# Kernel optimization log

Hardware: AMD Instinct MI355X
Metric: run time of the kernel (lower is better)

Reference implementation:

```python
import jax, jax.numpy as jnp
import numpy as np
import math

FACTOR = 5  # ProbAttention factor


def setup_inputs() -> dict:
    key = jax.random.key(0)
    kq, kk, kv = jax.random.split(key, 3)
    B, L, H, D = 4, 2048, 8, 64
    return {
        "queries": jax.random.normal(kq, (B, L, H, D), dtype=jnp.float32),
        "keys": jax.random.normal(kk, (B, L, H, D), dtype=jnp.float32),
        "values": jax.random.normal(kv, (B, L, H, D), dtype=jnp.float32),
    }


def reference(queries, keys, values):
    # queries/keys/values: [B, L, H, D] (self-attention, L == S)
    B, L, H, D = queries.shape
    S = keys.shape[1]
    Q = jnp.transpose(queries, (0, 2, 1, 3))  # [B,H,L,D]
    K = jnp.transpose(keys, (0, 2, 1, 3))     # [B,H,S,D]
    V = jnp.transpose(values, (0, 2, 1, 3))   # [B,H,S,D]

    # U: number of top queries kept; u: number of sampled keys per query
    n_top = min(max(1, int(FACTOR * math.log(max(S, 2)))), S, L)
    sample_k = min(max(1, int(FACTOR * math.log(max(L, 2)))), S)

    # --- _prob_QK: sampled QK, sparsity measure, top-k query selection ---
    idx_key = jax.random.key(42)  # matches torch.randint(L, (S, sample_k)) role
    index_sample = jax.random.randint(idx_key, (L, sample_k), 0, S)  # [L_Q, sample_k]
    K_sample = K[:, :, index_sample, :]                # [B,H,L,sample_k,D]
    QK_sample = jnp.einsum('bhqd,bhqjd->bhqj', Q, K_sample)  # [B,H,L,sample_k]
    # sparsity measure: max - mean (mean over full key length L_K = S)
    M = QK_sample.max(axis=-1) - QK_sample.sum(axis=-1) / S   # [B,H,L]
    M_top = jax.lax.top_k(M, n_top)[1]                 # [B,H,n_top] query indices
    Q_reduce = jnp.take_along_axis(Q, M_top[..., None], axis=2)  # [B,H,n_top,D]
    scores = jnp.einsum('bhud,bhkd->bhuk', Q_reduce, K)          # [B,H,n_top,S]

    scale = 1.0 / math.sqrt(D)
    scores = scores * scale

    # --- initial context: mask_flag=True and L_Q == L_V -> causal cumsum of V ---
    context = jnp.cumsum(V, axis=2)                    # [B,H,L,D]

    # --- masked softmax over selected queries (ProbMask: causal triu(1) rows) ---
    tri = jnp.triu(jnp.ones((S, S), dtype=bool), 1)    # [S,S]
    mask = tri[M_top]                                  # [B,H,n_top,S]
    scores = jnp.where(mask, -jnp.inf, scores)
    attn = jax.nn.softmax(scores, axis=-1)             # dropout is identity at eval
    attended = jnp.einsum('bhuk,bhkd->bhud', attn, V)  # [B,H,n_top,D]

    # --- scatter attended values into context at selected query positions ---
    b_idx = jnp.arange(B)[:, None, None]
    h_idx = jnp.arange(H)[None, :, None]
    context = context.at[b_idx, h_idx, M_top].set(attended)

    return jnp.transpose(context, (0, 2, 1, 3))        # [B,L,H,D]
```

## Files before the change

kernel.cpp:

```cpp
#include <hip/hip_runtime.h>
#include <hip/hip_bf16.h>
#include <math.h>

#define B_   4
#define L_   2048
#define H_   8
#define D_   64
#define NTOP 38
#define SAMPK 38


#define WS_M_OFF    0
#define WS_MTOP_OFF 262144
#define WS_SMALL    (WS_MTOP_OFF + 4864)
#define NSLOT16     (B_ * H_ * NTOP * 16)
#define WS16_PMAX   WS_SMALL
#define WS16_PSUM   (WS16_PMAX + NSLOT16 * 4)
#define WS16_PPV    (WS16_PSUM + NSLOT16 * 4)
#define WS16_TOTAL  (WS16_PPV + NSLOT16 * D_ * 4)

#define CHUNK16 128
#define SPITCH  132

__device__ __forceinline__ uint32_t rotl32(uint32_t v, int d) {
  return (v << d) | (v >> (32 - d));
}

__device__ __forceinline__ void threefry2x32(uint32_t k0, uint32_t k1,
                                             uint32_t x0, uint32_t x1,
                                             uint32_t& y0, uint32_t& y1) {
  const uint32_t ks2 = k0 ^ k1 ^ 0x1BD11BDAu;
  const uint32_t ks[3] = {k0, k1, ks2};
  x0 += k0; x1 += k1;
  const int ra[4] = {13, 15, 26, 6};
  const int rb[4] = {17, 29, 16, 24};
#pragma unroll
  for (int g = 0; g < 5; ++g) {
    const int* r = (g & 1) ? rb : ra;
#pragma unroll
    for (int i = 0; i < 4; ++i) {
      x0 += x1;
      x1 = rotl32(x1, r[i]);
      x1 ^= x0;
    }
    x0 += ks[(g + 1) % 3];
    x1 += ks[(g + 2) % 3] + (uint32_t)(g + 1);
  }
  y0 = x0; y1 = x1;
}

__device__ __forceinline__ int sample_idx(int t) {
  uint32_t k2_0, k2_1, y0, y1;
  threefry2x32(0u, 42u, 0u, 1u, k2_0, k2_1);
  threefry2x32(k2_0, k2_1, 0u, (uint32_t)t, y0, y1);
  return (int)((y0 ^ y1) & 2047u);
}

__device__ __forceinline__ int sample_idx_k2(uint32_t k2_0, uint32_t k2_1, int t) {
  uint32_t y0, y1;
  threefry2x32(k2_0, k2_1, 0u, (uint32_t)t, y0, y1);
  return (int)((y0 ^ y1) & 2047u);
}

__device__ __forceinline__ int argmax32_low(const float* __restrict__ vals,
                                            float& bv_out) {
  float t[16];
#pragma unroll
  for (int i = 0; i < 16; ++i) t[i] = fmaxf(vals[2 * i], vals[2 * i + 1]);
#pragma unroll
  for (int i = 0; i < 8; ++i) t[i] = fmaxf(t[2 * i], t[2 * i + 1]);
#pragma unroll
  for (int i = 0; i < 4; ++i) t[i] = fmaxf(t[2 * i], t[2 * i + 1]);
  float bv = fmaxf(fmaxf(t[0], t[1]), fmaxf(t[2], t[3]));
  uint32_t msk = 0u;
#pragma unroll
  for (int i = 0; i < 32; ++i)
    msk |= (vals[i] == bv) ? (1u << i) : 0u;
  bv_out = bv;
  return __ffs(msk) - 1;
}

__device__ __forceinline__ void topk38_wave_lds(const float* __restrict__ Mrow,
                                                int lane, int* __restrict__ spos,
                                                int* __restrict__ mtop_g, bool writeG) {
  float vals[32];
#pragma unroll
  for (int i = 0; i < 32; ++i)
    vals[i] = Mrow[lane + 64 * i];

  for (int u = 0; u < NTOP; ++u) {
    float bv;
    int bslot = argmax32_low(vals, bv);
    float v = bv;
    int idx = lane + 64 * bslot;
#pragma unroll
    for (int off = 1; off < 64; off <<= 1) {
      float v2 = __shfl_xor(v, off);
      int   i2 = __shfl_xor(idx, off);
      if (v2 > v || (v2 == v && i2 < idx)) { v = v2; idx = i2; }
    }
    if (lane == 0) {
      spos[u] = idx;
      if (writeG) mtop_g[u] = idx;
    }
    if ((idx & 63) == lane) {
      int slot = idx >> 6;
#pragma unroll
      for (int i = 0; i < 32; ++i)
        if (i == slot) vals[i] = -1e38f;
    }
  }
}

__device__ __forceinline__ void topk38_wave(const float* __restrict__ Mrow,
                                            int lane, int* __restrict__ mrow_out) {
  float vals[32];
#pragma unroll
  for (int i = 0; i < 32; ++i)
    vals[i] = Mrow[lane + 64 * i];

  for (int u = 0; u < NTOP; ++u) {
    float bv;
    int bslot = argmax32_low(vals, bv);
    float v = bv;
    int idx = lane + 64 * bslot;
#pragma unroll
    for (int off = 1; off < 64; off <<= 1) {
      float v2 = __shfl_xor(v, off);
      int   i2 = __shfl_xor(idx, off);
      if (v2 > v || (v2 == v && i2 < idx)) { v = v2; idx = i2; }
    }
    if (lane == 0) mrow_out[u] = idx;
    if ((idx & 63) == lane) {
      int slot = idx >> 6;
#pragma unroll
      for (int i = 0; i < 32; ++i)
        if (i == slot) vals[i] = -1e38f;
    }
  }
}

__global__ __launch_bounds__(256) void m_cumsum_kernel(const float* __restrict__ Q,
                                                       const float* __restrict__ K,
                                                       const float* __restrict__ V,
                                                       float* __restrict__ M,
                                                       float* __restrict__ out) {
  __shared__ uint16_t sidx[16][SAMPK];
  __shared__ float cs[8][32];

  int tid = threadIdx.x;

  if (blockIdx.x < 64) {
    int bI = blockIdx.x;
    int bh = bI >> 1, dhalf = bI & 1;
    int h = bh & (H_ - 1), b = bh >> 3;
    int dl = tid & 31, c = tid >> 5;
    const int CH = L_ / 8;
    int d = dhalf * 32 + dl;
    size_t base = ((size_t)b * L_ * H_ + h) * D_ + d;
    const size_t ls = (size_t)H_ * D_;
    float s = 0.f;
    for (int l = c * CH; l < (c + 1) * CH; ++l)
      s += V[base + (size_t)l * ls];
    cs[c][dl] = s;
    __syncthreads();
    float run = 0.f;
    for (int cc = 0; cc < c; ++cc) run += cs[cc][dl];
    for (int l = c * CH; l < (c + 1) * CH; ++l) {
      run += V[base + (size_t)l * ls];
      out[base + (size_t)l * ls] = run;
    }
    return;
  }

  int bI = blockIdx.x - 64;
  int j8 = bI >> 3;
  int bh = (bI & 7) + 8 * (j8 >> 7);
  int chunk = j8 & 127;
  int grp = tid >> 4, c = tid & 15;
  int q = chunk * 16 + grp;
  int h = bh & (H_ - 1), b = bh >> 3;

  {
    uint32_t k2_0, k2_1;
    threefry2x32(0u, 42u, 0u, 1u, k2_0, k2_1);
    for (int s = tid; s < 16 * SAMPK; s += 256) {
      int ql = s / SAMPK, jj = s - ql * SAMPK;
      sidx[ql][jj] =
          (uint16_t)sample_idx_k2(k2_0, k2_1, (chunk * 16 + ql) * SAMPK + jj);
    }
  }
  __syncthreads();

  float4 qv = *(const float4*)(Q + (((size_t)b * L_ + q) * H_ + h) * D_ + 4 * c);
  const float* Kbase = K + ((size_t)b * L_ * H_ + h) * D_ + 4 * c;

  float mx = -1e30f, smv = 0.f;
  int j = 0;
  for (; j + 4 <= SAMPK; j += 4) {
    int r0 = (int)sidx[grp][j];
    int r1 = (int)sidx[grp][j + 1];
    int r2 = (int)sidx[grp][j + 2];
    int r3 = (int)sidx[grp][j + 3];
    float4 k0 = *(const float4*)(Kbase + (size_t)r0 * (H_ * D_));
    float4 k1 = *(const float4*)(Kbase + (size_t)r1 * (H_ * D_));
    float4 k2 = *(const float4*)(Kbase + (size_t)r2 * (H_ * D_));
    float4 k3 = *(const float4*)(Kbase + (size_t)r3 * (H_ * D_));
    float p0 = qv.x * k0.x + qv.y * k0.y + qv.z * k0.z + qv.w * k0.w;
    float p1 = qv.x * k1.x + qv.y * k1.y + qv.z * k1.z + qv.w * k1.w;
    float p2 = qv.x * k2.x + qv.y * k2.y + qv.z * k2.z + qv.w * k2.w;
    float p3 = qv.x * k3.x + qv.y * k3.y + qv.z * k3.z + qv.w * k3.w;
#pragma unroll
    for (int off = 1; off < 16; off <<= 1) {
      p0 += __shfl_xor(p0, off);
      p1 += __shfl_xor(p1, off);
      p2 += __shfl_xor(p2, off);
      p3 += __shfl_xor(p3, off);
    }
    mx = fmaxf(mx, p0); smv += p0;
    mx = fmaxf(mx, p1); smv += p1;
    mx = fmaxf(mx, p2); smv += p2;
    mx = fmaxf(mx, p3); smv += p3;
  }
  for (; j < SAMPK; ++j) {
    int r0 = (int)sidx[grp][j];
    float4 k0 = *(const float4*)(Kbase + (size_t)r0 * (H_ * D_));
    float p0 = qv.x * k0.x + qv.y * k0.y + qv.z * k0.z + qv.w * k0.w;
#pragma unroll
    for (int off = 1; off < 16; off <<= 1)
      p0 += __shfl_xor(p0, off);
    mx = fmaxf(mx, p0); smv += p0;
  }
  if (c == 0)
    M[(size_t)bh * L_ + q] = mx - smv * (1.0f / (float)L_);
}

__global__ __launch_bounds__(512) void attn_split_tk_kernel(const float* __restrict__ Q,
                                                            const float* __restrict__ K,
                                                            const float* __restrict__ V,
                                                            const float* __restrict__ M,
                                                            int* __restrict__ mtop,
                                                            float* __restrict__ pmax,
                                                            float* __restrict__ psum,
                                                            float* __restrict__ ppv) {
  __shared__ float4 sK[CHUNK16 * 16];
  __shared__ float  sS[NTOP * SPITCH];
  __shared__ float4 sQ[NTOP * 16];
  __shared__ int    spos[NTOP];

  int bI = blockIdx.x;
  int c = bI & 15;
  int bh = bI >> 4;
  int h = bh & (H_ - 1), b = bh >> 3;
  int kstart = c * CHUNK16;
  int tid = threadIdx.x;

  const float* Kb = K + ((size_t)b * L_ * H_ + h) * D_;
  const float* Vb = V + ((size_t)b * L_ * H_ + h) * D_;
  const float* Qb = Q + ((size_t)b * L_ * H_ + h) * D_;

  if (tid < 64) {
    topk38_wave_lds(M + (size_t)bh * L_, tid, spos, mtop + bh * NTOP, c == 0);
  } else {
    for (int s = tid - 64; s < CHUNK16 * 16; s += 448) {
      int row = s >> 4, f = s & 15;
      sK[row * 16 + (f ^ (row & 15))] =
          *(const float4*)(Kb + (size_t)(kstart + row) * (H_ * D_) + 4 * f);
    }
  }
  __syncthreads();

  int maxpos = 0;
  for (int u = 0; u < NTOP; ++u) maxpos = max(maxpos, spos[u]);
  if (maxpos < kstart) return;

  for (int s = tid; s < NTOP * 16; s += 512) {
    int u = s >> 4, f = s & 15;
    sQ[s] = *(const float4*)(Qb + (size_t)spos[u] * (H_ * D_) + 4 * f);
  }
  __syncthreads();

  {
    int k = tid & 127;
    int ug = tid >> 7;
    float4 kreg[16];
#pragma unroll
    for (int f = 0; f < 16; ++f)
      kreg[f] = sK[k * 16 + (f ^ (k & 15))];

    int u0 = ug * 10, u1 = min(NTOP, u0 + 10);
    for (int u = u0; u < u1; ++u) {
      int pos = spos[u];
      if (pos < kstart) continue;
      int kloc = pos - kstart;
      float dot = 0.f;
#pragma unroll
      for (int f = 0; f < 16; ++f) {
        float4 qf = sQ[u * 16 + f];
        dot += kreg[f].x * qf.x + kreg[f].y * qf.y
             + kreg[f].z * qf.z + kreg[f].w * qf.w;
      }
      sS[u * SPITCH + k] = (k <= kloc) ? dot * 0.125f : -1e30f;
    }
  }
  __syncthreads();

  int w = tid >> 6, lane = tid & 63;
  int kq = lane >> 4, dq = lane & 15;
  for (int u = w; u < NTOP; u += 8) {
    int pos = spos[u];
    if (pos < kstart) continue;
    int kcnt = min(CHUNK16, pos + 1 - kstart);

    float s0 = sS[u * SPITCH + lane];
    float s1 = sS[u * SPITCH + 64 + lane];
    float m = fmaxf(s0, s1);
#pragma unroll
    for (int off = 1; off < 64; off <<= 1)
      m = fmaxf(m, __shfl_xor(m, off));
    float p0 = expf(s0 - m), p1 = expf(s1 - m);
    sS[u * SPITCH + lane] = p0;
    sS[u * SPITCH + 64 + lane] = p1;
    float sum = p0 + p1;
#pragma unroll
    for (int off = 1; off < 64; off <<= 1)
      sum += __shfl_xor(sum, off);

    float4 acc = make_float4(0.f, 0.f, 0.f, 0.f);
    for (int k0 = 0; k0 < kcnt; k0 += 4) {
      int kk = k0 + kq;
      if (kk < kcnt) {
        float p = sS[u * SPITCH + kk];
        float4 v4 = *(const float4*)(Vb + (size_t)(kstart + kk) * (H_ * D_) + 4 * dq);
        acc.x += p * v4.x; acc.y += p * v4.y;
        acc.z += p * v4.z; acc.w += p * v4.w;
      }
    }
    acc.x += __shfl_xor(acc.x, 16); acc.y += __shfl_xor(acc.y, 16);
    acc.z += __shfl_xor(acc.z, 16); acc.w += __shfl_xor(acc.w, 16);
    acc.x += __shfl_xor(acc.x, 32); acc.y += __shfl_xor(acc.y, 32);
    acc.z += __shfl_xor(acc.z, 32); acc.w += __shfl_xor(acc.w, 32);

    int slot = (bh * NTOP + u) * 16 + c;
    if (lane < 16)
      *(float4*)(ppv + (size_t)slot * D_ + 4 * lane) = acc;
    if (lane == 0) { pmax[slot] = m; psum[slot] = sum; }
  }
}

template <int NCHT>
__global__ __launch_bounds__(64) void attn_fin_kernel(const float* __restrict__ pmax,
                                                      const float* __restrict__ psum,
                                                      const float* __restrict__ ppv,
                                                      const int* __restrict__ mtop,
                                                      float* __restrict__ out) {
  const int CH = L_ / NCHT;
  int uu = blockIdx.x;
  int bh = uu / NTOP;
  int h = bh & (H_ - 1), b = bh >> 3;
  int pos = mtop[uu];
  if (pos < 0) pos = 0;
  if (pos > L_ - 1) pos = L_ - 1;
  int klen = pos + 1;
  int nch = (klen + CH - 1) / CH;
  int tid = threadIdx.x;

  int base = uu * NCHT;
  float gmax = -1e30f;
#pragma unroll
  for (int cc = 0; cc < NCHT; ++cc)
    if (cc < nch) gmax = fmaxf(gmax, pmax[base + cc]);

  float gsum = 0.f, acc = 0.f;
#pragma unroll
  for (int cc = 0; cc < NCHT; ++cc) {
    if (cc < nch) {
      float w0 = expf(pmax[base + cc] - gmax);
      gsum += psum[base + cc] * w0;
      acc += ppv[(size_t)(base + cc) * D_ + tid] * w0;
    }
  }
  out[(((size_t)b * L_ + pos) * H_ + h) * D_ + tid] = acc / gsum;
}

__global__ __launch_bounds__(256) void m_kernel(const float* __restrict__ Q,
                                                const float* __restrict__ K,
                                                float* __restrict__ M) {
  int bI = blockIdx.x;
  int j8 = bI >> 3;
  int bh = (bI & 7) + 8 * (j8 >> 7);
  int chunk = j8 & 127;
  int tid = threadIdx.x;
  int grp = tid >> 4, c = tid & 15;
  int q = chunk * 16 + grp;
  int h = bh & (H_ - 1), b = bh >> 3;

  __shared__ uint16_t sidx[16][SAMPK];
  for (int s = tid; s < 16 * SAMPK; s += 256) {
    int ql = s / SAMPK, jj = s - ql * SAMPK;
    sidx[ql][jj] = (uint16_t)sample_idx((chunk * 16 + ql) * SAMPK + jj);
  }
  __syncthreads();

  float4 qv = *(const float4*)(Q + (((size_t)b * L_ + q) * H_ + h) * D_ + 4 * c);
  const float* Kbase = K + ((size_t)b * L_ * H_ + h) * D_ + 4 * c;

  float mx = -1e30f, smv = 0.f;
  for (int j = 0; j < SAMPK; ++j) {
    int row = (int)sidx[grp][j];
    float4 kv = *(const float4*)(Kbase + (size_t)row * (H_ * D_));
    float part = qv.x * kv.x + qv.y * kv.y + qv.z * kv.z + qv.w * kv.w;
#pragma unroll
    for (int off = 1; off < 16; off <<= 1)
      part += __shfl_xor(part, off);
    mx = fmaxf(mx, part);
    smv += part;
  }
  if (c == 0)
    M[(size_t)bh * L_ + q] = mx - smv * (1.0f / (float)L_);
}

__global__ __launch_bounds__(1024) void cumsum_kernel(const float* __restrict__ V,
                                                      float* __restrict__ out) {
  int bI = blockIdx.x;
  int bh = bI >> 1, dhalf = bI & 1;
  int h = bh & (H_ - 1), b = bh >> 3;
  int tid = threadIdx.x;
  int dl = tid & 31, c = tid >> 5;
  int d = dhalf * 32 + dl;
  const int CH = L_ / 32;
  __shared__ float cs[32][32];
  size_t base = ((size_t)b * L_ * H_ + h) * D_ + d;
  const size_t ls = (size_t)H_ * D_;
  float s = 0.f;
  for (int l = c * CH; l < (c + 1) * CH; ++l)
    s += V[base + (size_t)l * ls];
  cs[c][dl] = s;
// ... 108 lines not shown
                                                    float* __restrict__ out) {
  int bh = blockIdx.x;
  int h = bh % H_, b = bh / H_;
  int tid = threadIdx.x;

  __shared__ float sm[L_];
  __shared__ float redv[256];
  __shared__ int   redi[256];
  __shared__ int   mtop_s[NTOP];
  __shared__ float qs[D_];
  __shared__ float part[4][D_];

  for (int q = tid; q < L_; q += 256) {
    const float4* q4 = (const float4*)(Q + (((size_t)b * L_ + q) * H_ + h) * D_);
    float4 qv[16];
#pragma unroll
    for (int i = 0; i < 16; ++i) qv[i] = q4[i];
    float mx = -1e30f, smv = 0.f;
    for (int j = 0; j < SAMPK; ++j) {
      int kk = sample_idx(q * SAMPK + j);
      const float4* k4 = (const float4*)(K + (((size_t)b * L_ + kk) * H_ + h) * D_);
      float dot = 0.f;
#pragma unroll
      for (int i = 0; i < 16; ++i) {
        float4 kv = k4[i];
        dot += qv[i].x * kv.x + qv[i].y * kv.y + qv[i].z * kv.z + qv[i].w * kv.w;
      }
      mx = fmaxf(mx, dot);
      smv += dot;
    }
    sm[q] = mx - smv * (1.0f / (float)L_);
  }
  __syncthreads();

  for (int u = 0; u < NTOP; ++u) {
    float bv = -1e38f; int bi = -1;
    for (int i = tid; i < L_; i += 256) {
      float v = sm[i];
      if (v > bv) { bv = v; bi = i; }
    }
    redv[tid] = bv; redi[tid] = bi;
    __syncthreads();
    for (int s = 128; s > 0; s >>= 1) {
      if (tid < s) {
        float v2 = redv[tid + s]; int i2 = redi[tid + s];
        if (v2 > redv[tid] ||
            (v2 == redv[tid] && i2 >= 0 && (redi[tid] < 0 || i2 < redi[tid]))) {
          redv[tid] = v2; redi[tid] = i2;
        }
      }
      __syncthreads();
    }
    if (tid == 0) {
      int sel = redi[0];
      if (sel < 0) sel = 0;
      mtop_s[u] = sel;
      sm[sel] = -1e38f;
    }
    __syncthreads();
  }

  for (int u = 0; u < NTOP; ++u) {
    int pos = mtop_s[u];
    if (pos < 0) pos = 0;
    if (pos > L_ - 1) pos = L_ - 1;
    int klen = pos + 1;

    __syncthreads();
    if (tid < D_)
      qs[tid] = Q[(((size_t)b * L_ + pos) * H_ + h) * D_ + tid];
    __syncthreads();

    float lmax = -1e30f;
    for (int k = tid; k < klen; k += 256) {
      const float4* k4 = (const float4*)(K + (((size_t)b * L_ + k) * H_ + h) * D_);
      float dot = 0.f;
#pragma unroll
      for (int i = 0; i < 16; ++i) {
        float4 kv = k4[i];
        dot += qs[4 * i] * kv.x + qs[4 * i + 1] * kv.y
             + qs[4 * i + 2] * kv.z + qs[4 * i + 3] * kv.w;
      }
      dot *= 0.125f;
      sm[k] = dot;
      lmax = fmaxf(lmax, dot);
    }
    redv[tid] = lmax;
    __syncthreads();
    for (int s = 128; s > 0; s >>= 1) {
      if (tid < s) redv[tid] = fmaxf(redv[tid], redv[tid + s]);
      __syncthreads();
    }
    float mx = redv[0];
    __syncthreads();

    float lsum = 0.f;
    for (int k = tid; k < klen; k += 256) {
      float p = expf(sm[k] - mx);
      sm[k] = p;
      lsum += p;
    }
    redv[tid] = lsum;
    __syncthreads();
    for (int s = 128; s > 0; s >>= 1) {
      if (tid < s) redv[tid] += redv[tid + s];
      __syncthreads();
    }
    float inv = 1.0f / redv[0];
    __syncthreads();

    int d = tid & 63, slice = tid >> 6;
    float acc = 0.f;
    for (int k = slice; k < klen; k += 4)
      acc += sm[k] * V[(((size_t)b * L_ + k) * H_ + h) * D_ + d];
    part[slice][d] = acc;
    __syncthreads();
    if (tid < D_) {
      float r = (part[0][tid] + part[1][tid]) + (part[2][tid] + part[3][tid]);
      out[(((size_t)b * L_ + pos) * H_ + h) * D_ + tid] = r * inv;
    }
  }
}

extern "C" void kernel_launch(void* const* d_in, const int* in_sizes, int n_in,
                              void* d_out, int out_size, void* d_ws, size_t ws_size,
                              hipStream_t stream) {
  const float* Q = (const float*)d_in[0];
  const float* K = (const float*)d_in[1];
  const float* V = (const float*)d_in[2];
  float* out = (float*)d_out;

  if (ws_size >= (size_t)WS16_TOTAL) {
    char* ws = (char*)d_ws;
    float* M    = (float*)(ws + WS_M_OFF);
    int*   mt   = (int*)(ws + WS_MTOP_OFF);
    float* pmax = (float*)(ws + WS16_PMAX);
    float* psum = (float*)(ws + WS16_PSUM);
    float* ppv  = (float*)(ws + WS16_PPV);

    m_cumsum_kernel<<<4160, 256, 0, stream>>>(Q, K, V, M, out);
    attn_split_tk_kernel<<<B_ * H_ * 16, 512, 0, stream>>>(Q, K, V, M, mt,
                                                           pmax, psum, ppv);
    attn_fin_kernel<16><<<B_ * H_ * NTOP, 64, 0, stream>>>(pmax, psum, ppv, mt, out);
  } else if (ws_size >= (size_t)WS_SMALL) {
    char* ws = (char*)d_ws;
    float* M  = (float*)(ws + WS_M_OFF);
    int*   mt = (int*)(ws + WS_MTOP_OFF);

    m_kernel<<<4096, 256, 0, stream>>>(Q, K, M);
    topk_reg_kernel<<<B_ * H_, 64, 0, stream>>>(M, mt);
    cumsum_kernel<<<B_ * H_ * 2, 1024, 0, stream>>>(V, out);
    attn_kernel<<<B_ * H_ * NTOP, 256, 0, stream>>>(Q, K, V, mt, out);
  } else {
    cumsum_kernel<<<B_ * H_ * 2, 1024, 0, stream>>>(V, out);
    fused_kernel<<<B_ * H_, 256, 0, stream>>>(Q, K, V, out);
  }
}
```

Measured before the change: 200.2 us.

## Fuse all stages into one cooperative kernel with grid-wide syncs

Adds a persistent cooperative mega-kernel that runs cumsum, sampled-QK sparsity scoring, top-k selection, split-K attention over 64-key chunks and the final merge in a single launch, with grid.sync between phases. It removes the cost of three separate kernel launches and the gaps between them. The attention split also changes from 16 to 32 chunks, and chunks entirely beyond the largest selected position are skipped. In exchange, grid-wide barriers add overhead, most blocks sit idle during the top-k phase, and the path only runs when 1024 blocks of 512 threads can be co-resident, otherwise it falls back to the old kernels.

Measured after the change: 201.5 us. About the same (+0.6%).

```diff
diff --git a/kernel.cpp b/kernel.cpp
--- a/kernel.cpp
+++ b/kernel.cpp
@@ -1,6 +1,9 @@
 #include <hip/hip_runtime.h>
 #include <hip/hip_bf16.h>
+#include <hip/hip_cooperative_groups.h>
 #include <math.h>
+
+namespace cg = cooperative_groups;
 
 #define B_   4
 #define L_   2048
@@ -18,9 +21,17 @@
 #define WS16_PSUM   (WS16_PMAX + NSLOT16 * 4)
 #define WS16_PPV    (WS16_PSUM + NSLOT16 * 4)
 #define WS16_TOTAL  (WS16_PPV + NSLOT16 * D_ * 4)
+#define NSLOT32     (B_ * H_ * NTOP * 32)
+#define WS32_PMAX   WS_SMALL
+#define WS32_PSUM   (WS32_PMAX + NSLOT32 * 4)
+#define WS32_PPV    (WS32_PSUM + NSLOT32 * 4)
+#define WS32_TOTAL  (WS32_PPV + NSLOT32 * D_ * 4)
 
 #define CHUNK16 128
 #define SPITCH  132
+#define CHM     64
+#define NCHM    32
+#define SPM     68
 
 __device__ __forceinline__ uint32_t rotl32(uint32_t v, int d) {
   return (v << d) | (v >> (32 - d));
@@ -80,9 +91,8 @@
   return __ffs(msk) - 1;
 }
 
-__device__ __forceinline__ void topk38_wave_lds(const float* __restrict__ Mrow,
-                                                int lane, int* __restrict__ spos,
-                                                int* __restrict__ mtop_g, bool writeG) {
+__device__ __forceinline__ void topk38_wave(const float* __restrict__ Mrow,
+                                            int lane, int* __restrict__ mrow_out) {
   float vals[32];
 #pragma unroll
   for (int i = 0; i < 32; ++i)
@@ -99,10 +109,7 @@
       int   i2 = __shfl_xor(idx, off);
       if (v2 > v || (v2 == v && i2 < idx)) { v = v2; idx = i2; }
     }
-    if (lane == 0) {
-      spos[u] = idx;
-      if (writeG) mtop_g[u] = idx;
-    }
+    if (lane == 0) mrow_out[u] = idx;
     if ((idx & 63) == lane) {
       int slot = idx >> 6;
 #pragma unroll
@@ -112,8 +119,9 @@
   }
 }
 
-__device__ __forceinline__ void topk38_wave(const float* __restrict__ Mrow,
-                                            int lane, int* __restrict__ mrow_out) {
+__device__ __forceinline__ void topk38_wave_lds(const float* __restrict__ Mrow,
+                                                int lane, int* __restrict__ spos,
+                                                int* __restrict__ mtop_g, bool writeG) {
   float vals[32];
 #pragma unroll
   for (int i = 0; i < 32; ++i)
@@ -130,12 +138,246 @@
       int   i2 = __shfl_xor(idx, off);
       if (v2 > v || (v2 == v && i2 < idx)) { v = v2; idx = i2; }
     }
-    if (lane == 0) mrow_out[u] = idx;
+    if (lane == 0) {
+      spos[u] = idx;
+      if (writeG) mtop_g[u] = idx;
+    }
     if ((idx & 63) == lane) {
       int slot = idx >> 6;
 #pragma unroll
       for (int i = 0; i < 32; ++i)
         if (i == slot) vals[i] = -1e38f;
+    }
+  }
+}
+
+struct SharedA {
+  uint16_t sidx[2][16][SAMPK];
+  float    cs[2][8][32];
+};
+struct SharedC {
+  float4 sK[CHM * 16];
+  float  sS[NTOP * SPM];
+  float4 sQ[NTOP * 16];
+  int    spos[NTOP];
+};
+union SharedU { SharedA a; SharedC c; };
+
+__global__ __launch_bounds__(512, 8) void mega_kernel(
+    const float* __restrict__ Q, const float* __restrict__ K,
+    const float* __restrict__ V, float* __restrict__ M,
+    int* __restrict__ mtop, float* __restrict__ pmax,
+    float* __restrict__ psum, float* __restrict__ ppv,
+    float* __restrict__ out) {
+  cg::grid_group grid = cg::this_grid();
+  __shared__ SharedU sh;
+
+  int bI = blockIdx.x;
+  int tid = threadIdx.x;
+  int half = tid >> 8, htid = tid & 255;
+
+  if (bI < 32) {
+    int unit = bI * 2 + half;
+    int bh = unit >> 1, dhalf = unit & 1;
+    int h = bh & (H_ - 1), b = bh >> 3;
+    int dl = htid & 31, cc8 = htid >> 5;
+    const int CH = L_ / 8;
+    int d = dhalf * 32 + dl;
+    size_t base = ((size_t)b * L_ * H_ + h) * D_ + d;
+    const size_t ls = (size_t)H_ * D_;
+    float s = 0.f;
+    for (int l = cc8 * CH; l < (cc8 + 1) * CH; ++l)
+      s += V[base + (size_t)l * ls];
+    sh.a.cs[half][cc8][dl] = s;
+    __syncthreads();
+    float run = 0.f;
+    for (int c2 = 0; c2 < cc8; ++c2) run += sh.a.cs[half][c2][dl];
+    for (int l = cc8 * CH; l < (cc8 + 1) * CH; ++l) {
+      run += V[base + (size_t)l * ls];
+      out[base + (size_t)l * ls] = run;
+    }
+  }
+
+  {
+    uint32_t k2_0, k2_1;
+    threefry2x32(0u, 42u, 0u, 1u, k2_0, k2_1);
+    for (int r = 0; r < 2; ++r) {
+      int um = (bI & 7) + 8 * (((bI >> 3) * 2 + half) * 2 + r);
+      int j8 = um >> 3;
+      int bh = (um & 7) + 8 * (j8 >> 7);
+      int chunk = j8 & 127;
+      int grp = htid >> 4, c = htid & 15;
+      int q = chunk * 16 + grp;
+      int h = bh & (H_ - 1), b = bh >> 3;
+
+      __syncthreads();
+      for (int s = htid; s < 16 * SAMPK; s += 256) {
+        int ql = s / SAMPK, jj = s - ql * SAMPK;
+        sh.a.sidx[half][ql][jj] =
+            (uint16_t)sample_idx_k2(k2_0, k2_1, (chunk * 16 + ql) * SAMPK + jj);
+      }
+      __syncthreads();
+
+      float4 qv = *(const float4*)(Q + (((size_t)b * L_ + q) * H_ + h) * D_ + 4 * c);
+      const float* Kbase = K + ((size_t)b * L_ * H_ + h) * D_ + 4 * c;
+
+      float mx = -1e30f, smv = 0.f;
+      int j = 0;
+      for (; j + 4 <= SAMPK; j += 4) {
+        int r0 = (int)sh.a.sidx[half][grp][j];
+        int r1 = (int)sh.a.sidx[half][grp][j + 1];
+        int r2 = (int)sh.a.sidx[half][grp][j + 2];
+        int r3 = (int)sh.a.sidx[half][grp][j + 3];
+        float4 k0 = *(const float4*)(Kbase + (size_t)r0 * (H_ * D_));
+        float4 k1 = *(const float4*)(Kbase + (size_t)r1 * (H_ * D_));
+        float4 k2 = *(const float4*)(Kbase + (size_t)r2 * (H_ * D_));
+        float4 k3 = *(const float4*)(Kbase + (size_t)r3 * (H_ * D_));
+        float p0 = qv.x * k0.x + qv.y * k0.y + qv.z * k0.z + qv.w * k0.w;
+        float p1 = qv.x * k1.x + qv.y * k1.y + qv.z * k1.z + qv.w * k1.w;
+        float p2 = qv.x * k2.x + qv.y * k2.y + qv.z * k2.z + qv.w * k2.w;
+        float p3 = qv.x * k3.x + qv.y * k3.y + qv.z * k3.z + qv.w * k3.w;
+#pragma unroll
+        for (int off = 1; off < 16; off <<= 1) {
+          p0 += __shfl_xor(p0, off);
+          p1 += __shfl_xor(p1, off);
+          p2 += __shfl_xor(p2, off);
+          p3 += __shfl_xor(p3, off);
+        }
+        mx = fmaxf(mx, p0); smv += p0;
+        mx = fmaxf(mx, p1); smv += p1;
+        mx = fmaxf(mx, p2); smv += p2;
+        mx = fmaxf(mx, p3); smv += p3;
+      }
+      for (; j < SAMPK; ++j) {
+        int r0 = (int)sh.a.sidx[half][grp][j];
+        float4 k0 = *(const float4*)(Kbase + (size_t)r0 * (H_ * D_));
+        float p0 = qv.x * k0.x + qv.y * k0.y + qv.z * k0.z + qv.w * k0.w;
+#pragma unroll
+        for (int off = 1; off < 16; off <<= 1)
+          p0 += __shfl_xor(p0, off);
+        mx = fmaxf(mx, p0); smv += p0;
+      }
+      if (c == 0)
+        M[(size_t)bh * L_ + q] = mx - smv * (1.0f / (float)L_);
+    }
+  }
+  grid.sync();
+
+  if (bI >= 32 && bI < 64 && tid < 64)
+    topk38_wave(M + (size_t)(bI - 32) * L_, tid, mtop + (bI - 32) * NTOP);
+  grid.sync();
+
+  {
+    int bh = (bI & 7) + 8 * (bI >> 8);
+    int c = (bI >> 3) & 31;
+    int h = bh & (H_ - 1), b = bh >> 3;
+    int kstart = c * CHM;
+
+    if (tid < NTOP) sh.c.spos[tid] = mtop[bh * NTOP + tid];
+    __syncthreads();
+    int maxpos = 0;
+    for (int u = 0; u < NTOP; ++u) maxpos = max(maxpos, sh.c.spos[u]);
+
+    if (maxpos >= kstart) {
+      const float* Kb = K + ((size_t)b * L_ * H_ + h) * D_;
+      const float* Vb = V + ((size_t)b * L_ * H_ + h) * D_;
+      const float* Qb = Q + ((size_t)b * L_ * H_ + h) * D_;
+
+      for (int s = tid; s < CHM * 16; s += 512) {
+        int row = s >> 4, f = s & 15;
+        sh.c.sK[row * 16 + (f ^ (row & 15))] =
+            *(const float4*)(Kb + (size_t)(kstart + row) * (H_ * D_) + 4 * f);
+      }
+      for (int s = tid; s < NTOP * 16; s += 512) {
+        int u = s >> 4, f = s & 15;
+        sh.c.sQ[s] = *(const float4*)(Qb + (size_t)sh.c.spos[u] * (H_ * D_) + 4 * f);
+      }
+      __syncthreads();
+
+      {
+        int k = tid & 63, ug = tid >> 6;
+        float4 kreg[16];
+#pragma unroll
+        for (int f = 0; f < 16; ++f)
+          kreg[f] = sh.c.sK[k * 16 + (f ^ (k & 15))];
+        for (int u = ug; u < NTOP; u += 8) {
+          int pos = sh.c.spos[u];
+          if (pos < kstart) continue;
+          float dot = 0.f;
+#pragma unroll
+          for (int f = 0; f < 16; ++f) {
+            float4 qf = sh.c.sQ[u * 16 + f];
+            dot += kreg[f].x * qf.x + kreg[f].y * qf.y
+                 + kreg[f].z * qf.z + kreg[f].w * qf.w;
+          }
+          sh.c.sS[u * SPM + k] = (k <= pos - kstart) ? dot * 0.125f : -1e30f;
+        }
+      }
+      __syncthreads();
+
+      {
+        int w = tid >> 6, lane = tid & 63;
+        int kq = lane >> 4, dq = lane & 15;
+        for (int u = w; u < NTOP; u += 8) {
+          int pos = sh.c.spos[u];
+          if (pos < kstart) continue;
+          int kcnt = min(CHM, pos + 1 - kstart);
+          float s0 = sh.c.sS[u * SPM + lane];
+          float m = s0;
+#pragma unroll
+          for (int off = 1; off < 64; off <<= 1)
+            m = fmaxf(m, __shfl_xor(m, off));
+          float p0 = expf(s0 - m);
+          sh.c.sS[u * SPM + lane] = p0;
+          float sum = p0;
+#pragma unroll
+          for (int off = 1; off < 64; off <<= 1)
+            sum += __shfl_xor(sum, off);
+
+          float4 acc = make_float4(0.f, 0.f, 0.f, 0.f);
+          for (int k0 = 0; k0 < kcnt; k0 += 4) {
+            int kk = k0 + kq;
+            if (kk < kcnt) {
+              float p = sh.c.sS[u * SPM + kk];
+              float4 v4 = *(const float4*)(Vb + (size_t)(kstart + kk) * (H_ * D_) + 4 * dq);
+              acc.x += p * v4.x; acc.y += p * v4.y;
+              acc.z += p * v4.z; acc.w += p * v4.w;
+            }
+          }
+          acc.x += __shfl_xor(acc.x, 16); acc.y += __shfl_xor(acc.y, 16);
+          acc.z += __shfl_xor(acc.z, 16); acc.w += __shfl_xor(acc.w, 16);
+          acc.x += __shfl_xor(acc.x, 32); acc.y += __shfl_xor(acc.y, 32);
+          acc.z += __shfl_xor(acc.z, 32); acc.w += __shfl_xor(acc.w, 32);
+
+          int slot = (bh * NTOP + u) * NCHM + c;
+          if (lane < 16)
+            *(float4*)(ppv + (size_t)slot * D_ + 4 * lane) = acc;
+          if (lane == 0) { pmax[slot] = m; psum[slot] = sum; }
+        }
+      }
+    }
+  }
+  grid.sync();
+
+  {
+    int wid = bI * 8 + (tid >> 6);
+    int lane = tid & 63;
+    if (wid < B_ * H_ * NTOP) {
+      int bh = wid / NTOP;
+      int h = bh & (H_ - 1), b = bh >> 3;
+      int pos = mtop[wid];
+      int nch = (pos + CHM) / CHM;
+      int base = wid * NCHM;
+      float gmax = -1e30f;
+      for (int cc = 0; cc < nch; ++cc)
+        gmax = fmaxf(gmax, pmax[base + cc]);
+      float gsum = 0.f, acc = 0.f;
+      for (int cc = 0; cc < nch; ++cc) {
+        float w0 = expf(pmax[base + cc] - gmax);
+        gsum += psum[base + cc] * w0;
+        acc += ppv[(size_t)(base + cc) * D_ + lane] * w0;
+      }
+      out[(((size_t)b * L_ + pos) * H_ + h) * D_ + lane] = acc / gsum;
     }
   }
 }
@@ -675,6 +917,38 @@
   const float* V = (const float*)d_in[2];
   float* out = (float*)d_out;
 
+  if (ws_size >= (size_t)WS32_TOTAL) {
+    static int coop = -1;
+    if (coop < 0) {
+      int dev = 0;
+      (void)hipGetDevice(&dev);
+      int attr = 0;
+      (void)hipDeviceGetAttribute(&attr, hipDeviceAttributeCooperativeLaunch, dev);
+      int nb = 0;
+      hipError_t oe =
+          hipOccupancyMaxActiveBlocksPerMultiprocessor(&nb, mega_kernel, 512, 0);
+      hipDeviceProp_t prop;
+      hipError_t pe = hipGetDeviceProperties(&prop, dev);
+      coop = (attr && oe == hipSuccess && pe == hipSuccess &&
+              (long)nb * prop.multiProcessorCount >= 1024) ? 1 : 0;
+    }
+    if (coop == 1) {
+      char* ws = (char*)d_ws;
+      float* M    = (float*)(ws + WS_M_OFF);
+      int*   mt   = (int*)(ws + WS_MTOP_OFF);
+      float* pmax = (float*)(ws + WS32_PMAX);
+      float* psum = (float*)(ws + WS32_PSUM);
+      float* ppv  = (float*)(ws + WS32_PPV);
+      void* args[] = {(void*)&Q, (void*)&K, (void*)&V, (void*)&M, (void*)&mt,
+                      (void*)&pmax, (void*)&psum, (void*)&ppv, (void*)&out};
+      hipError_t e = hipLaunchCooperativeKernel(mega_kernel, dim3(1024), dim3(512),
+                                                args, 0, stream);
+      if (e == hipSuccess) return;
+      (void)hipGetLastError();
+      coop = 0;
+    }
+  }
+
   if (ws_size >= (size_t)WS16_TOTAL) {
     char* ws = (char*)d_ws;
     float* M    = (float*)(ws + WS_M_OFF);
```

## Split keys into 32 chunks and pair early/late chunks per block for causal balance

Applied to the files above, without the earlier changes.

Adds an attention path that splits each head's keys into 32 chunks of 64 and assigns each block a pair of chunks (j and 31-j), so causal-mask work is balanced across blocks instead of later chunks sitting idle or exiting early. Top-k selection still runs once per block but its cost is now amortized over two chunks, and the finalize kernel merges 32 partials. The workspace grows to hold twice as many partial slots, and the QK stage now reads K from LDS per dot product instead of caching it in registers. The new path is used whenever the workspace is large enough, otherwise the previous 16-chunk path runs.

Measured after the change: 207.9 us. +3.8%, slower.

```diff
diff --git a/kernel.cpp b/kernel.cpp
--- a/kernel.cpp
+++ b/kernel.cpp
@@ -18,9 +18,17 @@
 #define WS16_PSUM   (WS16_PMAX + NSLOT16 * 4)
 #define WS16_PPV    (WS16_PSUM + NSLOT16 * 4)
 #define WS16_TOTAL  (WS16_PPV + NSLOT16 * D_ * 4)
+#define NSLOT32     (B_ * H_ * NTOP * 32)
+#define WS32_PMAX   WS_SMALL
+#define WS32_PSUM   (WS32_PMAX + NSLOT32 * 4)
+#define WS32_PPV    (WS32_PSUM + NSLOT32 * 4)
+#define WS32_TOTAL  (WS32_PPV + NSLOT32 * D_ * 4)
 
 #define CHUNK16 128
 #define SPITCH  132
+#define CHM     64
+#define NCHM    32
+#define SPM     68
 
 __device__ __forceinline__ uint32_t rotl32(uint32_t v, int d) {
   return (v << d) | (v >> (32 - d));
@@ -80,9 +88,8 @@
   return __ffs(msk) - 1;
 }
 
-__device__ __forceinline__ void topk38_wave_lds(const float* __restrict__ Mrow,
-                                                int lane, int* __restrict__ spos,
-                                                int* __restrict__ mtop_g, bool writeG) {
+__device__ __forceinline__ void topk38_wave(const float* __restrict__ Mrow,
+                                            int lane, int* __restrict__ mrow_out) {
   float vals[32];
 #pragma unroll
   for (int i = 0; i < 32; ++i)
@@ -99,10 +106,7 @@
       int   i2 = __shfl_xor(idx, off);
       if (v2 > v || (v2 == v && i2 < idx)) { v = v2; idx = i2; }
     }
-    if (lane == 0) {
-      spos[u] = idx;
-      if (writeG) mtop_g[u] = idx;
-    }
+    if (lane == 0) mrow_out[u] = idx;
     if ((idx & 63) == lane) {
       int slot = idx >> 6;
 #pragma unroll
@@ -112,8 +116,9 @@
   }
 }
 
-__device__ __forceinline__ void topk38_wave(const float* __restrict__ Mrow,
-                                            int lane, int* __restrict__ mrow_out) {
+__device__ __forceinline__ void topk38_wave_lds(const float* __restrict__ Mrow,
+                                                int lane, int* __restrict__ spos,
+                                                int* __restrict__ mtop_g, bool writeG) {
   float vals[32];
 #pragma unroll
   for (int i = 0; i < 32; ++i)
@@ -130,7 +135,10 @@
       int   i2 = __shfl_xor(idx, off);
       if (v2 > v || (v2 == v && i2 < idx)) { v = v2; idx = i2; }
     }
-    if (lane == 0) mrow_out[u] = idx;
+    if (lane == 0) {
+      spos[u] = idx;
+      if (writeG) mtop_g[u] = idx;
+    }
     if ((idx & 63) == lane) {
       int slot = idx >> 6;
 #pragma unroll
@@ -235,24 +243,23 @@
     M[(size_t)bh * L_ + q] = mx - smv * (1.0f / (float)L_);
 }
 
-__global__ __launch_bounds__(512) void attn_split_tk_kernel(const float* __restrict__ Q,
-                                                            const float* __restrict__ K,
-                                                            const float* __restrict__ V,
-                                                            const float* __restrict__ M,
-                                                            int* __restrict__ mtop,
-                                                            float* __restrict__ pmax,
-                                                            float* __restrict__ psum,
-                                                            float* __restrict__ ppv) {
-  __shared__ float4 sK[CHUNK16 * 16];
-  __shared__ float  sS[NTOP * SPITCH];
+__global__ __launch_bounds__(512) void attn_pair_tk_kernel(const float* __restrict__ Q,
+                                                           const float* __restrict__ K,
+                                                           const float* __restrict__ V,
+                                                           const float* __restrict__ M,
+                                                           int* __restrict__ mtop,
+                                                           float* __restrict__ pmax,
+                                                           float* __restrict__ psum,
+                                                           float* __restrict__ ppv) {
+  __shared__ float4 sK[CHM * 16];
+  __shared__ float  sS[NTOP * SPM];
   __shared__ float4 sQ[NTOP * 16];
   __shared__ int    spos[NTOP];
 
   int bI = blockIdx.x;
-  int c = bI & 15;
-  int bh = bI >> 4;
+  int bh = (bI & 7) + 8 * (bI >> 7);
+  int jj = (bI >> 3) & 15;
   int h = bh & (H_ - 1), b = bh >> 3;
-  int kstart = c * CHUNK16;
   int tid = threadIdx.x;
 
   const float* Kb = K + ((size_t)b * L_ * H_ + h) * D_;
@@ -260,91 +267,99 @@
   const float* Qb = Q + ((size_t)b * L_ * H_ + h) * D_;
 
   if (tid < 64) {
-    topk38_wave_lds(M + (size_t)bh * L_, tid, spos, mtop + bh * NTOP, c == 0);
+    topk38_wave_lds(M + (size_t)bh * L_, tid, spos, mtop + bh * NTOP, jj == 0);
   } else {
-    for (int s = tid - 64; s < CHUNK16 * 16; s += 448) {
+    int kstart0 = jj * CHM;
+    for (int s = tid - 64; s < CHM * 16; s += 448) {
       int row = s >> 4, f = s & 15;
       sK[row * 16 + (f ^ (row & 15))] =
-          *(const float4*)(Kb + (size_t)(kstart + row) * (H_ * D_) + 4 * f);
+          *(const float4*)(Kb + (size_t)(kstart0 + row) * (H_ * D_) + 4 * f);
     }
   }
   __syncthreads();
 
   int maxpos = 0;
   for (int u = 0; u < NTOP; ++u) maxpos = max(maxpos, spos[u]);
-  if (maxpos < kstart) return;
 
   for (int s = tid; s < NTOP * 16; s += 512) {
     int u = s >> 4, f = s & 15;
     sQ[s] = *(const float4*)(Qb + (size_t)spos[u] * (H_ * D_) + 4 * f);
   }
-  __syncthreads();
-
-  {
-    int k = tid & 127;
-    int ug = tid >> 7;
-    float4 kreg[16];
-#pragma unroll
-    for (int f = 0; f < 16; ++f)
-      kreg[f] = sK[k * 16 + (f ^ (k & 15))];
-
-    int u0 = ug * 10, u1 = min(NTOP, u0 + 10);
-    for (int u = u0; u < u1; ++u) {
-      int pos = spos[u];
-      if (pos < kstart) continue;
-      int kloc = pos - kstart;
-      float dot = 0.f;
-#pragma unroll
-      for (int f = 0; f < 16; ++f) {
-        float4 qf = sQ[u * 16 + f];
-        dot += kreg[f].x * qf.x + kreg[f].y * qf.y
-             + kreg[f].z * qf.z + kreg[f].w * qf.w;
+
+  for (int ph = 0; ph < 2; ++ph) {
+    int c = ph ? (31 - jj) : jj;
+    int kstart = c * CHM;
+    if (maxpos < kstart) continue;
+
+    __syncthreads();
+
+    if (ph == 1) {
+      for (int s = tid; s < CHM * 16; s += 512) {
+        int row = s >> 4, f = s & 15;
+        sK[row * 16 + (f ^ (row & 15))] =
+            *(const float4*)(Kb + (size_t)(kstart + row) * (H_ * D_) + 4 * f);
       }
-      sS[u * SPITCH + k] = (k <= kloc) ? dot * 0.125f : -1e30f;
-    }
-  }
-  __syncthreads();
-
-  int w = tid >> 6, lane = tid & 63;
-  int kq = lane >> 4, dq = lane & 15;
-  for (int u = w; u < NTOP; u += 8) {
-    int pos = spos[u];
-    if (pos < kstart) continue;
-    int kcnt = min(CHUNK16, pos + 1 - kstart);
-
-    float s0 = sS[u * SPITCH + lane];
-    float s1 = sS[u * SPITCH + 64 + lane];
-    float m = fmaxf(s0, s1);
-#pragma unroll
-    for (int off = 1; off < 64; off <<= 1)
-      m = fmaxf(m, __shfl_xor(m, off));
-    float p0 = expf(s0 - m), p1 = expf(s1 - m);
-    sS[u * SPITCH + lane] = p0;
-    sS[u * SPITCH + 64 + lane] = p1;
-    float sum = p0 + p1;
-#pragma unroll
-    for (int off = 1; off < 64; off <<= 1)
-      sum += __shfl_xor(sum, off);
-
-    float4 acc = make_float4(0.f, 0.f, 0.f, 0.f);
-    for (int k0 = 0; k0 < kcnt; k0 += 4) {
-      int kk = k0 + kq;
-      if (kk < kcnt) {
-        float p = sS[u * SPITCH + kk];
-        float4 v4 = *(const float4*)(Vb + (size_t)(kstart + kk) * (H_ * D_) + 4 * dq);
-        acc.x += p * v4.x; acc.y += p * v4.y;
-        acc.z += p * v4.z; acc.w += p * v4.w;
+      __syncthreads();
+    }
+
+    {
+      int k = tid & 63, ug = tid >> 6;
+      for (int u = ug; u < NTOP; u += 8) {
+        int pos = spos[u];
+        if (pos < kstart) continue;
+        int kloc = pos - kstart;
+        float dot = 0.f;
+#pragma unroll
+        for (int f = 0; f < 16; ++f) {
+          float4 kv = sK[k * 16 + (f ^ (k & 15))];
+          float4 qf = sQ[u * 16 + f];
+          dot += kv.x * qf.x + kv.y * qf.y + kv.z * qf.z + kv.w * qf.w;
+        }
+        sS[u * SPM + k] = (k <= kloc) ? dot * 0.125f : -1e30f;
       }
     }
-    acc.x += __shfl_xor(acc.x, 16); acc.y += __shfl_xor(acc.y, 16);
-    acc.z += __shfl_xor(acc.z, 16); acc.w += __shfl_xor(acc.w, 16);
-    acc.x += __shfl_xor(acc.x, 32); acc.y += __shfl_xor(acc.y, 32);
-    acc.z += __shfl_xor(acc.z, 32); acc.w += __shfl_xor(acc.w, 32);
-
-    int slot = (bh * NTOP + u) * 16 + c;
-    if (lane < 16)
-      *(float4*)(ppv + (size_t)slot * D_ + 4 * lane) = acc;
-    if (lane == 0) { pmax[slot] = m; psum[slot] = sum; }
+    __syncthreads();
+
+    {
+      int w = tid >> 6, lane = tid & 63;
+      int kq = lane >> 4, dq = lane & 15;
+      for (int u = w; u < NTOP; u += 8) {
+        int pos = spos[u];
+        if (pos < kstart) continue;
+        int kcnt = min(CHM, pos + 1 - kstart);
+        float s0 = sS[u * SPM + lane];
+        float m = s0;
+#pragma unroll
+        for (int off = 1; off < 64; off <<= 1)
+          m = fmaxf(m, __shfl_xor(m, off));
+        float p0 = expf(s0 - m);
+        sS[u * SPM + lane] = p0;
+        float sum = p0;
+#pragma unroll
+        for (int off = 1; off < 64; off <<= 1)
+          sum += __shfl_xor(sum, off);
+
+        float4 acc = make_float4(0.f, 0.f, 0.f, 0.f);
+        for (int k0 = 0; k0 < kcnt; k0 += 4) {
+          int kk = k0 + kq;
+          if (kk < kcnt) {
+            float p = sS[u * SPM + kk];
+            float4 v4 = *(const float4*)(Vb + (size_t)(kstart + kk) * (H_ * D_) + 4 * dq);
+            acc.x += p * v4.x; acc.y += p * v4.y;
+            acc.z += p * v4.z; acc.w += p * v4.w;
+          }
+        }
+        acc.x += __shfl_xor(acc.x, 16); acc.y += __shfl_xor(acc.y, 16);
+        acc.z += __shfl_xor(acc.z, 16); acc.w += __shfl_xor(acc.w, 16);
+        acc.x += __shfl_xor(acc.x, 32); acc.y += __shfl_xor(acc.y, 32);
+        acc.z += __shfl_xor(acc.z, 32); acc.w += __shfl_xor(acc.w, 32);
+
+        int slot = (bh * NTOP + u) * NCHM + c;
+        if (lane < 16)
+          *(float4*)(ppv + (size_t)slot * D_ + 4 * lane) = acc;
+        if (lane == 0) { pmax[slot] = m; psum[slot] = sum; }
+      }
+    }
   }
 }
 
@@ -383,6 +398,119 @@
   out[(((size_t)b * L_ + pos) * H_ + h) * D_ + tid] = acc / gsum;
 }
 
+__global__ __launch_bounds__(512) void attn_split_tk_kernel(const float* __restrict__ Q,
+                                                            const float* __restrict__ K,
+                                                            const float* __restrict__ V,
+                                                            const float* __restrict__ M,
+                                                            int* __restrict__ mtop,
+                                                            float* __restrict__ pmax,
+                                                            float* __restrict__ psum,
+                                                            float* __restrict__ ppv) {
+  __shared__ float4 sK[CHUNK16 * 16];
+  __shared__ float  sS[NTOP * SPITCH];
+  __shared__ float4 sQ[NTOP * 16];
+  __shared__ int    spos[NTOP];
+
+  int bI = blockIdx.x;
+  int c = bI & 15;
+  int bh = bI >> 4;
+  int h = bh & (H_ - 1), b = bh >> 3;
+  int kstart = c * CHUNK16;
+  int tid = threadIdx.x;
+
+  const float* Kb = K + ((size_t)b * L_ * H_ + h) * D_;
+  const float* Vb = V + ((size_t)b * L_ * H_ + h) * D_;
+  const float* Qb = Q + ((size_t)b * L_ * H_ + h) * D_;
+
+  if (tid < 64) {
+    topk38_wave_lds(M + (size_t)bh * L_, tid, spos, mtop + bh * NTOP, c == 0);
+  } else {
+    for (int s = tid - 64; s < CHUNK16 * 16; s += 448) {
+      int row = s >> 4, f = s & 15;
+      sK[row * 16 + (f ^ (row & 15))] =
+          *(const float4*)(Kb + (size_t)(kstart + row) * (H_ * D_) + 4 * f);
+    }
+  }
+  __syncthreads();
+
+  int maxpos = 0;
+  for (int u = 0; u < NTOP; ++u) maxpos = max(maxpos, spos[u]);
+  if (maxpos < kstart) return;
+
+  for (int s = tid; s < NTOP * 16; s += 512) {
+    int u = s >> 4, f = s & 15;
+    sQ[s] = *(const float4*)(Qb + (size_t)spos[u] * (H_ * D_) + 4 * f);
+  }
+  __syncthreads();
+
+  {
+    int k = tid & 127;
+    int ug = tid >> 7;
+    float4 kreg[16];
+#pragma unroll
+    for (int f = 0; f < 16; ++f)
+      kreg[f] = sK[k * 16 + (f ^ (k & 15))];
+
+    int u0 = ug * 10, u1 = min(NTOP, u0 + 10);
+    for (int u = u0; u < u1; ++u) {
+      int pos = spos[u];
+      if (pos < kstart) continue;
+      int kloc = pos - kstart;
+      float dot = 0.f;
+#pragma unroll
+      for (int f = 0; f < 16; ++f) {
+        float4 qf = sQ[u * 16 + f];
+        dot += kreg[f].x * qf.x + kreg[f].y * qf.y
+             + kreg[f].z * qf.z + kreg[f].w * qf.w;
+      }
+      sS[u * SPITCH + k] = (k <= kloc) ? dot * 0.125f : -1e30f;
+    }
+  }
+  __syncthreads();
+
+  int w = tid >> 6, lane = tid & 63;
+  int kq = lane >> 4, dq = lane & 15;
+  for (int u = w; u < NTOP; u += 8) {
+    int pos = spos[u];
+    if (pos < kstart) continue;
+    int kcnt = min(CHUNK16, pos + 1 - kstart);
+
+    float s0 = sS[u * SPITCH + lane];
+    float s1 = sS[u * SPITCH + 64 + lane];
+    float m = fmaxf(s0, s1);
+#pragma unroll
+    for (int off = 1; off < 64; off <<= 1)
+      m = fmaxf(m, __shfl_xor(m, off));
+    float p0 = expf(s0 - m), p1 = expf(s1 - m);
+    sS[u * SPITCH + lane] = p0;
+    sS[u * SPITCH + 64 + lane] = p1;
+    float sum = p0 + p1;
+#pragma unroll
+    for (int off = 1; off < 64; off <<= 1)
+      sum += __shfl_xor(sum, off);
+
+    float4 acc = make_float4(0.f, 0.f, 0.f, 0.f);
+    for (int k0 = 0; k0 < kcnt; k0 += 4) {
+      int kk = k0 + kq;
+      if (kk < kcnt) {
+        float p = sS[u * SPITCH + kk];
+        float4 v4 = *(const float4*)(Vb + (size_t)(kstart + kk) * (H_ * D_) + 4 * dq);
+        acc.x += p * v4.x; acc.y += p * v4.y;
+        acc.z += p * v4.z; acc.w += p * v4.w;
+      }
+    }
+    acc.x += __shfl_xor(acc.x, 16); acc.y += __shfl_xor(acc.y, 16);
+    acc.z += __shfl_xor(acc.z, 16); acc.w += __shfl_xor(acc.w, 16);
+    acc.x += __shfl_xor(acc.x, 32); acc.y += __shfl_xor(acc.y, 32);
+    acc.z += __shfl_xor(acc.z, 32); acc.w += __shfl_xor(acc.w, 32);
+
+    int slot = (bh * NTOP + u) * 16 + c;
+    if (lane < 16)
+      *(float4*)(ppv + (size_t)slot * D_ + 4 * lane) = acc;
+    if (lane == 0) { pmax[slot] = m; psum[slot] = sum; }
+  }
+}
+
 __global__ __launch_bounds__(256) void m_kernel(const float* __restrict__ Q,
                                                 const float* __restrict__ K,
                                                 float* __restrict__ M) {
@@ -675,7 +803,18 @@
   const float* V = (const float*)d_in[2];
   float* out = (float*)d_out;
 
-  if (ws_size >= (size_t)WS16_TOTAL) {
+  if (ws_size >= (size_t)WS32_TOTAL) {
+    char* ws = (char*)d_ws;
+    float* M    = (float*)(ws + WS_M_OFF);
+    int*   mt   = (int*)(ws + WS_MTOP_OFF);
+    float* pmax = (float*)(ws + WS32_PMAX);
+    float* psum = (float*)(ws + WS32_PSUM);
+    float* ppv  = (float*)(ws + WS32_PPV);
+
+    m_cumsum_kernel<<<4160, 256, 0, stream>>>(Q, K, V, M, out);
+    attn_pair_tk_kernel<<<512, 512, 0, stream>>>(Q, K, V, M, mt, pmax, psum, ppv);
+    attn_fin_kernel<NCHM><<<B_ * H_ * NTOP, 64, 0, stream>>>(pmax, psum, ppv, mt, out);
+  } else if (ws_size >= (size_t)WS16_TOTAL) {
     char* ws = (char*)d_ws;
     float* M    = (float*)(ws + WS_M_OFF);
     int*   mt   = (int*)(ws + WS_MTOP_OFF);
```

## Replace wave-serial top-k with block-wide radix select in attention split kernel

Applied to the files above, without the earlier changes.

The 38-step wave-level iterative argmax top-k is replaced by a 512-thread radix select over order-preserving uint keys. It builds per-wave LDS histograms over four 8-bit passes, then compacts and ranks the selected indices. K chunk loading now happens after selection, so blocks that early-exit skip it, but it no longer overlaps with the top-k. This adds many __syncthreads and atomics, and the 16 chunk blocks per head still each redo the selection.

Result: no change. 198.2 us (-1.0%).

```diff
diff --git a/kernel.cpp b/kernel.cpp
--- a/kernel.cpp
+++ b/kernel.cpp
@@ -80,9 +80,8 @@
   return __ffs(msk) - 1;
 }
 
-__device__ __forceinline__ void topk38_wave_lds(const float* __restrict__ Mrow,
-                                                int lane, int* __restrict__ spos,
-                                                int* __restrict__ mtop_g, bool writeG) {
+__device__ __forceinline__ void topk38_wave(const float* __restrict__ Mrow,
+                                            int lane, int* __restrict__ mrow_out) {
   float vals[32];
 #pragma unroll
   for (int i = 0; i < 32; ++i)
@@ -99,37 +98,6 @@
       int   i2 = __shfl_xor(idx, off);
       if (v2 > v || (v2 == v && i2 < idx)) { v = v2; idx = i2; }
     }
-    if (lane == 0) {
-      spos[u] = idx;
-      if (writeG) mtop_g[u] = idx;
-    }
-    if ((idx & 63) == lane) {
-      int slot = idx >> 6;
-#pragma unroll
-      for (int i = 0; i < 32; ++i)
-        if (i == slot) vals[i] = -1e38f;
-    }
-  }
-}
-
-__device__ __forceinline__ void topk38_wave(const float* __restrict__ Mrow,
-                                            int lane, int* __restrict__ mrow_out) {
-  float vals[32];
-#pragma unroll
-  for (int i = 0; i < 32; ++i)
-    vals[i] = Mrow[lane + 64 * i];
-
-  for (int u = 0; u < NTOP; ++u) {
-    float bv;
-    int bslot = argmax32_low(vals, bv);
-    float v = bv;
-    int idx = lane + 64 * bslot;
-#pragma unroll
-    for (int off = 1; off < 64; off <<= 1) {
-      float v2 = __shfl_xor(v, off);
-      int   i2 = __shfl_xor(idx, off);
-      if (v2 > v || (v2 == v && i2 < idx)) { v = v2; idx = i2; }
-    }
     if (lane == 0) mrow_out[u] = idx;
     if ((idx & 63) == lane) {
       int slot = idx >> 6;
@@ -138,6 +106,98 @@
         if (i == slot) vals[i] = -1e38f;
     }
   }
+}
+
+__device__ __forceinline__ void topk38_block512(const float* __restrict__ Mrow,
+                                                int tid,
+                                                uint32_t* __restrict__ keys,
+                                                uint32_t* __restrict__ whist,
+                                                uint32_t* __restrict__ hist,
+                                                int* __restrict__ sel,
+                                                int* __restrict__ cnts,
+                                                uint32_t* __restrict__ prsh,
+                                                int* __restrict__ spos,
+                                                int* __restrict__ mtop_g, bool writeG) {
+  int wv = tid >> 6;
+  for (int i = tid; i < L_; i += 512) {
+    uint32_t u = __float_as_uint(Mrow[i]);
+    keys[i] = (u & 0x80000000u) ? ~u : (u | 0x80000000u);
+  }
+  uint32_t prefix = 0u, remaining = NTOP;
+  for (int level = 24; level >= 0; level -= 8) {
+    for (int i = tid; i < 2048; i += 512) whist[i] = 0u;
+    __syncthreads();
+    uint32_t mask = (level == 24) ? 0u : (0xFFFFFFFFu << (level + 8));
+    for (int i = tid; i < L_; i += 512) {
+      uint32_t k = keys[i];
+      if ((k & mask) == prefix)
+        atomicAdd(&whist[wv * 256 + ((k >> level) & 255u)], 1u);
+    }
+    __syncthreads();
+    if (tid < 256) {
+      uint32_t s = 0u;
+#pragma unroll
+      for (int w2 = 0; w2 < 8; ++w2) s += whist[w2 * 256 + tid];
+      hist[tid] = s;
+    }
+    __syncthreads();
+    if (tid == 0) {
+      uint32_t cnt = 0u; int bsel = 0;
+      for (int bb = 255; bb >= 0; --bb) {
+        uint32_t cc = hist[bb];
+        if (cnt + cc >= remaining) { bsel = bb; break; }
+        cnt += cc;
+      }
+      prsh[0] = prefix | ((uint32_t)bsel << level);
+      prsh[1] = remaining - cnt;
+    }
+    __syncthreads();
+    prefix = prsh[0]; remaining = prsh[1];
+  }
+  uint32_t T = prefix;
+  int need_ties = (int)remaining;
+  uint32_t* tiebuf = whist;
+  if (tid == 0) { cnts[0] = 0; cnts[1] = 0; }
+  __syncthreads();
+  for (int i = tid; i < L_; i += 512) {
+    uint32_t k = keys[i];
+    if (k > T) {
+      int s = atomicAdd(&cnts[0], 1);
+      sel[s] = i;
+    } else if (k == T) {
+      int s = atomicAdd(&cnts[1], 1);
+      tiebuf[s] = (uint32_t)i;
+    }
+  }
+  __syncthreads();
+  int nAbove = cnts[0];
+  int nTie = cnts[1];
+  if (nTie == need_ties) {
+    if (tid < need_ties) sel[nAbove + tid] = (int)tiebuf[tid];
+  } else {
+    for (int i = tid; i < nTie; i += 512) {
+      uint32_t my = tiebuf[i];
+      int rank = 0;
+      for (int j2 = 0; j2 < nTie; ++j2)
+        rank += (tiebuf[j2] < my) ? 1 : 0;
+      if (rank < need_ties) sel[nAbove + rank] = (int)my;
+    }
+  }
+  __syncthreads();
+  if (tid < NTOP) {
+    int myidx = sel[tid];
+    uint32_t myk = keys[myidx];
+    int rank = 0;
+#pragma unroll
+    for (int j2 = 0; j2 < NTOP; ++j2) {
+      int oidx = sel[j2];
+      uint32_t ok = keys[oidx];
+      rank += ((ok > myk) || (ok == myk && oidx < myidx)) ? 1 : 0;
+    }
+    spos[rank] = myidx;
+    if (writeG) mtop_g[rank] = myidx;
+  }
+  __syncthreads();
 }
 
 __global__ __launch_bounds__(256) void m_cumsum_kernel(const float* __restrict__ Q,
@@ -247,6 +307,9 @@
   __shared__ float  sS[NTOP * SPITCH];
   __shared__ float4 sQ[NTOP * 16];
   __shared__ int    spos[NTOP];
+  __shared__ int    sel[40];
+  __shared__ int    cnts[2];
+  __shared__ uint32_t prsh[2];
 
   int bI = blockIdx.x;
   int c = bI & 15;
@@ -259,21 +322,23 @@
   const float* Vb = V + ((size_t)b * L_ * H_ + h) * D_;
   const float* Qb = Q + ((size_t)b * L_ * H_ + h) * D_;
 
-  if (tid < 64) {
-    topk38_wave_lds(M + (size_t)bh * L_, tid, spos, mtop + bh * NTOP, c == 0);
-  } else {
-    for (int s = tid - 64; s < CHUNK16 * 16; s += 448) {
-      int row = s >> 4, f = s & 15;
-      sK[row * 16 + (f ^ (row & 15))] =
-          *(const float4*)(Kb + (size_t)(kstart + row) * (H_ * D_) + 4 * f);
-    }
-  }
-  __syncthreads();
+  {
+    uint32_t* keys  = (uint32_t*)sS;
+    uint32_t* whist = (uint32_t*)sS + 2048;
+    uint32_t* hist  = (uint32_t*)sS + 4096;
+    topk38_block512(M + (size_t)bh * L_, tid, keys, whist, hist, sel, cnts, prsh,
+                    spos, mtop + bh * NTOP, c == 0);
+  }
 
   int maxpos = 0;
   for (int u = 0; u < NTOP; ++u) maxpos = max(maxpos, spos[u]);
   if (maxpos < kstart) return;
 
+  for (int s = tid; s < CHUNK16 * 16; s += 512) {
+    int row = s >> 4, f = s & 15;
+    sK[row * 16 + (f ^ (row & 15))] =
+        *(const float4*)(Kb + (size_t)(kstart + row) * (H_ * D_) + 4 * f);
+  }
   for (int s = tid; s < NTOP * 16; s += 512) {
     int u = s >> 4, f = s & 15;
     sQ[s] = *(const float4*)(Qb + (size_t)spos[u] * (H_ * D_) + 4 * f);
@@ -597,10 +662,10 @@
       __syncthreads();
     }
     if (tid == 0) {
-      int sel = redi[0];
-      if (sel < 0) sel = 0;
-      mtop_s[u] = sel;
-      sm[sel] = -1e38f;
+      int sel2 = redi[0];
+      if (sel2 < 0) sel2 = 0;
+      mtop_s[u] = sel2;
+      sm[sel2] = -1e38f;
     }
     __syncthreads();
   }
```
